# Kernel tuning notes

Hardware: AMD Instinct MI355X
Metric: run time of the kernel (lower is better)

Reference implementation:

```python
import jax, jax.numpy as jnp
import numpy as np

LEN = 20_000_000  # samples per channel (interleaved real/imag), divisible by 10


def setup_inputs() -> dict:
    key = jax.random.key(0)
    k0, k1, k2, k3 = jax.random.split(key, 4)
    in0 = jax.random.normal(k0, (LEN,), dtype=jnp.float32)
    in1 = jax.random.normal(k1, (LEN,), dtype=jnp.float32)
    in2 = jax.random.normal(k2, (LEN,), dtype=jnp.float32)
    in3 = jax.random.normal(k3, (LEN,), dtype=jnp.float32)
    # bf buffer: ones with imaginary parts (odd indices) zeroed
    bf = jnp.ones((1, 8), dtype=jnp.float32).at[0, 1::2].set(0.0)
    return {"in0": in0, "in1": in1, "in2": in2, "in3": in3, "bf": bf}


def reference(in0, in1, in2, in3, bf):
    # Deinterleave real/imag, stack channels -> (4, N), reshape to (B, 4, 5)
    in_real = jnp.stack((in0[::2], in1[::2], in2[::2], in3[::2]), axis=0).reshape(-1, 4, 5)
    in_imag = jnp.stack((in0[1::2], in1[1::2], in2[1::2], in3[1::2]), axis=0).reshape(-1, 4, 5)
    bf_real = bf[0, ::2].reshape(1, 1, 4)
    bf_imag = bf[0, 1::2].reshape(1, 1, 4)
    # Complex matmul: (1,1,4) @ (B,4,5) -> (B,1,5)
    out_real = jnp.matmul(bf_real, in_real) - jnp.matmul(bf_imag, in_imag)
    out_imag = jnp.matmul(bf_imag, in_real) + jnp.matmul(bf_real, in_imag)
    result = jnp.concatenate([out_real, out_imag], axis=2)  # (B,1,10)
    # Faithful to original: strided scatter on dim 1 (size 1) -> no-op copy
    result2 = jnp.zeros_like(result)
    result2 = result2.at[:, ::2].set(result[:, :5])
    result2 = result2.at[:, 1::2].set(result[:, 5:])
    return result2
```

## Files before the change

### kernel.cpp

```cpp
#include <hip/hip_runtime.h>
#include <hip/hip_bf16.h>


__global__ __launch_bounds__(256) void beamform_kernel(
    const float* __restrict__ in0, const float* __restrict__ in1,
    const float* __restrict__ in2, const float* __restrict__ in3,
    const float* __restrict__ bf, float* __restrict__ out,
    int blocksPerChannel, int threadsPerChannel)
{
    const int tid = blockIdx.x * blockDim.x + threadIdx.x;
    if (tid >= threadsPerChannel) return;
    const int ch = blockIdx.y;

    const float* __restrict__ in =
        (ch == 0) ? in0 : (ch == 1) ? in1 : (ch == 2) ? in2 : in3;

    const int bl = tid / 5;
    const int c  = tid - bl * 5;

    const float2* __restrict__ p =
        reinterpret_cast<const float2*>(in + (size_t)bl * 40 + 2 * c);
    const float2 x0 = p[0];
    const float2 x1 = p[5];
    const float2 x2 = p[10];
    const float2 x3 = p[15];

    const float br0 = bf[0], bi0 = bf[1];
    const float br1 = bf[2], bi1 = bf[3];
    const float br2 = bf[4], bi2 = bf[5];
    const float br3 = bf[6], bi3 = bf[7];

    float re = br0 * x0.x - bi0 * x0.y;
    float im = bi0 * x0.x + br0 * x0.y;
    re += br1 * x1.x - bi1 * x1.y;
    im += bi1 * x1.x + br1 * x1.y;
    re += br2 * x2.x - bi2 * x2.y;
    im += bi2 * x2.x + br2 * x2.y;
    re += br3 * x3.x - bi3 * x3.y;
    im += bi3 * x3.x + br3 * x3.y;

    const size_t b = (size_t)ch * blocksPerChannel + bl;
    float* __restrict__ o = out + b * 10;
    o[c] = re;
    o[5 + c] = im;
}

extern "C" void kernel_launch(void* const* d_in, const int* in_sizes, int n_in,
                              void* d_out, int out_size, void* d_ws, size_t ws_size,
                              hipStream_t stream)
{
    const float* in0 = (const float*)d_in[0];
    const float* in1 = (const float*)d_in[1];
    const float* in2 = (const float*)d_in[2];
    const float* in3 = (const float*)d_in[3];
    const float* bf  = (const float*)d_in[4];
    float* out = (float*)d_out;

    const int len = in_sizes[0];
    const int blocksPerChannel = len / 40;
    const int threadsPerChannel = blocksPerChannel * 5;

    const int block = 256;
    dim3 grid((threadsPerChannel + block - 1) / block, 4, 1);
    beamform_kernel<<<grid, dim3(block, 1, 1), 0, stream>>>(
        in0, in1, in2, in3, bf, out, blocksPerChannel, threadsPerChannel);
}
```

Measured before the change: 291.6 us.

## Stage inputs and outputs through swizzled LDS for fully coalesced float4 I/O

```diff
diff --git a/kernel.cpp b/kernel.cpp
--- a/kernel.cpp
+++ b/kernel.cpp
@@ -1,48 +1,108 @@
 #include <hip/hip_runtime.h>
-#include <hip/hip_bf16.h>
 
 
-__global__ __launch_bounds__(256) void beamform_kernel(
+constexpr int UNITS   = 256;
+constexpr int THREADS = 256;
+
+__global__ __launch_bounds__(THREADS) void beamform_kernel(
     const float* __restrict__ in0, const float* __restrict__ in1,
     const float* __restrict__ in2, const float* __restrict__ in3,
     const float* __restrict__ bf, float* __restrict__ out,
-    int blocksPerChannel, int threadsPerChannel)
+    int blocksPerChannel)
 {
-    const int tid = blockIdx.x * blockDim.x + threadIdx.x;
-    if (tid >= threadsPerChannel) return;
-    const int ch = blockIdx.y;
+    __shared__ float4 lds4[UNITS * 10];
+
+    const int tid    = threadIdx.x;
+    const int ch     = blockIdx.y;
+    const int wgBase = blockIdx.x * UNITS;
+    const int validUnits = min(UNITS, blocksPerChannel - wgBase);
 
     const float* __restrict__ in =
         (ch == 0) ? in0 : (ch == 1) ? in1 : (ch == 2) ? in2 : in3;
+    const float4* __restrict__ g4 =
+        reinterpret_cast<const float4*>(in) + (size_t)wgBase * 10;
 
-    const int bl = tid / 5;
-    const int c  = tid - bl * 5;
+    const float4 blo = reinterpret_cast<const float4*>(bf)[0];
+    const float4 bhi = reinterpret_cast<const float4*>(bf)[1];
+    const float br[4] = {blo.x, blo.z, bhi.x, bhi.z};
+    const float bi[4] = {blo.y, blo.w, bhi.y, bhi.w};
 
-    const float2* __restrict__ p =
-        reinterpret_cast<const float2*>(in + (size_t)bl * 40 + 2 * c);
-    const float2 x0 = p[0];
-    const float2 x1 = p[5];
-    const float2 x2 = p[10];
-    const float2 x3 = p[15];
+    if (validUnits == UNITS) {
+        float4 v[10];
+        #pragma unroll
+        for (int k = 0; k < 10; ++k)
+            v[k] = g4[k * THREADS + tid];
+        #pragma unroll
+        for (int k = 0; k < 10; ++k) {
+            const int i = k * THREADS + tid;
+            lds4[i ^ ((i / 10) & 7)] = v[k];
+        }
+    } else {
+        const int nf4 = validUnits * 10;
+        #pragma unroll
+        for (int k = 0; k < 10; ++k) {
+            const int i = k * THREADS + tid;
+            if (i < nf4) {
+                const float4 v = g4[i];
+                lds4[i ^ ((i / 10) & 7)] = v;
+            }
+        }
+    }
+    __syncthreads();
 
-    const float br0 = bf[0], bi0 = bf[1];
-    const float br1 = bf[2], bi1 = bf[3];
-    const float br2 = bf[4], bi2 = bf[5];
-    const float br3 = bf[6], bi3 = bf[7];
+    float re[5] = {0.f, 0.f, 0.f, 0.f, 0.f};
+    float im[5] = {0.f, 0.f, 0.f, 0.f, 0.f};
+    const bool active = (tid < validUnits);
+    if (active) {
+        #pragma unroll
+        for (int k = 0; k < 10; ++k) {
+            const float4 w = lds4[(tid * 10 + k) ^ (tid & 7)];
+            const float e[4] = {w.x, w.y, w.z, w.w};
+            #pragma unroll
+            for (int q = 0; q < 4; ++q) {
+                const int f   = 4 * k + q;
+                const int r   = f / 10;
+                const int rem = f - 10 * r;
+                const int c   = rem >> 1;
+                if ((rem & 1) == 0) {
+                    re[c] += br[r] * e[q];
+                    im[c] += bi[r] * e[q];
+                } else {
+                    re[c] -= bi[r] * e[q];
+                    im[c] += br[r] * e[q];
+                }
+            }
+        }
+    }
+    __syncthreads();
 
-    float re = br0 * x0.x - bi0 * x0.y;
-    float im = bi0 * x0.x + br0 * x0.y;
-    re += br1 * x1.x - bi1 * x1.y;
-    im += bi1 * x1.x + br1 * x1.y;
-    re += br2 * x2.x - bi2 * x2.y;
-    im += bi2 * x2.x + br2 * x2.y;
-    re += br3 * x3.x - bi3 * x3.y;
-    im += bi3 * x3.x + br3 * x3.y;
+    float2* lds2 = reinterpret_cast<float2*>(lds4);
+    if (active) {
+        lds2[tid * 5 + 0] = make_float2(re[0], re[1]);
+        lds2[tid * 5 + 1] = make_float2(re[2], re[3]);
+        lds2[tid * 5 + 2] = make_float2(re[4], im[0]);
+        lds2[tid * 5 + 3] = make_float2(im[1], im[2]);
+        lds2[tid * 5 + 4] = make_float2(im[3], im[4]);
+    }
+    __syncthreads();
 
-    const size_t b = (size_t)ch * blocksPerChannel + bl;
-    float* __restrict__ o = out + b * 10;
-    o[c] = re;
-    o[5 + c] = im;
+    float2* __restrict__ gout2 =
+        reinterpret_cast<float2*>(out) +
+        ((size_t)ch * blocksPerChannel + wgBase) * 5;
+    const int nf2 = validUnits * 5;
+    if (nf2 == UNITS * 5) {
+        #pragma unroll
+        for (int k = 0; k < 5; ++k) {
+            const int i = k * THREADS + tid;
+            gout2[i] = lds2[i];
+        }
+    } else {
+        #pragma unroll
+        for (int k = 0; k < 5; ++k) {
+            const int i = k * THREADS + tid;
+            if (i < nf2) gout2[i] = lds2[i];
+        }
+    }
 }
 
 extern "C" void kernel_launch(void* const* d_in, const int* in_sizes, int n_in,
@@ -58,10 +118,8 @@
 
     const int len = in_sizes[0];
     const int blocksPerChannel = len / 40;
-    const int threadsPerChannel = blocksPerChannel * 5;
 
-    const int block = 256;
-    dim3 grid((threadsPerChannel + block - 1) / block, 4, 1);
-    beamform_kernel<<<grid, dim3(block, 1, 1), 0, stream>>>(
-        in0, in1, in2, in3, bf, out, blocksPerChannel, threadsPerChannel);
+    dim3 grid((blocksPerChannel + UNITS - 1) / UNITS, 4, 1);
+    beamform_kernel<<<grid, dim3(THREADS, 1, 1), 0, stream>>>(
+        in0, in1, in2, in3, bf, out, blocksPerChannel);
 }
```

Measured after the change: 296.5 us. No clear change (+1.7%).
